# Kernel optimization log

Hardware: AMD Instinct MI355X
Metric: run time of the kernel (lower is better)

## Reference

```python
import jax, jax.numpy as jnp
import numpy as np

E = 256        # HP.EMBED_SIZE
R = 8          # number of derivation rules / MLPs
S = 512        # number of sequential derivation steps
N = 256        # nodes produced per step
N_INIT = 1024  # initial axiom (thax) embeddings
TOTAL = N_INIT + S * N  # 132096 rows in the vectors buffer
M = 65536      # masked nodes fed to eval_net


def setup_inputs() -> dict:
    key = jax.random.key(0)
    ks = jax.random.split(key, 12)
    rng = np.random.default_rng(0)

    init_vecs = jax.random.normal(ks[0], (N_INIT, E), jnp.float32)
    # rule MLPs: concat(2 parents) -> E (relu) -> E
    W1 = jax.random.normal(ks[1], (R, 2 * E, E), jnp.float32) * (1.0 / np.sqrt(2 * E))
    b1 = jnp.zeros((R, E), jnp.float32)
    W2 = jax.random.normal(ks[2], (R, E, E), jnp.float32) * (1.0 / np.sqrt(E))
    b2 = jnp.zeros((R, E), jnp.float32)
    # eval net: E -> E (relu) -> 1
    eval_W1 = jax.random.normal(ks[3], (E, E), jnp.float32) * (1.0 / np.sqrt(E))
    eval_b1 = jnp.zeros((E,), jnp.float32)
    eval_W2 = jax.random.normal(ks[4], (E, 1), jnp.float32) * (1.0 / np.sqrt(E))
    eval_b2 = jnp.zeros((1,), jnp.float32)

    # step s writes rows [N_INIT + s*N, N_INIT + (s+1)*N)
    ind_steps = (N_INIT + np.arange(S * N, dtype=np.int32)).reshape(S, N)
    # parents drawn causally from already-computed prefix [0, N_INIT + s*N)
    highs = (N_INIT + np.arange(S, dtype=np.int64) * N)[:, None, None]
    pars_ind_steps = (rng.random((S, N, 2)) * highs).astype(np.int32)
    rule_steps = rng.integers(0, R, size=(S,)).astype(np.int32)
    mask = rng.integers(0, TOTAL, size=(M,)).astype(np.int32)

    pos = jax.random.uniform(ks[5], (M,), jnp.float32)
    neg = jax.random.uniform(ks[6], (M,), jnp.float32)
    target = jnp.round(jax.random.uniform(ks[7], (M,), jnp.float32))

    return {
        'init_vecs': init_vecs, 'W1': W1, 'b1': b1, 'W2': W2, 'b2': b2,
        'eval_W1': eval_W1, 'eval_b1': eval_b1, 'eval_W2': eval_W2, 'eval_b2': eval_b2,
        'pos': pos, 'neg': neg, 'target': target,
        'ind_steps': jnp.asarray(ind_steps), 'pars_ind_steps': jnp.asarray(pars_ind_steps),
        'rule_steps': jnp.asarray(rule_steps), 'mask': jnp.asarray(mask),
    }


def reference(init_vecs, W1, b1, W2, b2, eval_W1, eval_b1, eval_W2, eval_b2,
              pos, neg, target, ind_steps, pars_ind_steps, rule_steps, mask):
    vectors = jnp.zeros((TOTAL, E), init_vecs.dtype).at[:N_INIT].set(init_vecs)

    def step(vec, xs):
        inds, pars, r = xs            # [N], [N,2], scalar rule id
        p = vec[pars].reshape(N, 2 * E)   # gather parents
        h = jax.nn.relu(p @ W1[r] + b1[r])
        out = h @ W2[r] + b2[r]
        return vec.at[inds].set(out), None  # scatter new node embeddings

    vectors, _ = jax.lax.scan(step, vectors, (ind_steps, pars_ind_steps, rule_steps))

    x = vectors[mask]
    val = (jax.nn.relu(x @ eval_W1 + eval_b1) @ eval_W2 + eval_b2)[:, 0]

    # pos_weight = POS_WEIGHT_EXTRA * tot_neg / tot_pos (constant w.r.t. grads)
    pw = jax.lax.stop_gradient(jnp.sum(neg) / jnp.maximum(jnp.sum(pos), 1.0))
    # BCEWithLogitsLoss(pos_weight, reduction='none')
    contrib = pw * target * jax.nn.softplus(-val) + (1.0 - target) * jax.nn.softplus(val)
    loss = jnp.sum((pos + neg) * contrib)
    posOK = jnp.sum(pos * (val >= 0))
    negOK = jnp.sum(neg * (val < 0))
    return loss, posOK, negOK
```

## Files before the change

kernel.cpp:

```cpp
#include <hip/hip_runtime.h>
#include <math.h>

#define EMB   256
#define TWOE  512
#define NINIT 1024
#define NSTEP 512
#define NPS   256
#define TOTAL (NINIT + NSTEP * NPS)
#define MM    65536
#define NNODE (NSTEP * NPS)
#define NKEY  2048
#define BTH   512
#define TROWS 32
#define CHK_SH  16384
#define RULE_SH (24 * CHK_SH)

typedef short s16x8 __attribute__((ext_vector_type(8)));
typedef float f32x4 __attribute__((ext_vector_type(4)));

#define OFF_VECH   0ull
#define OFF_VECL   ((size_t)TOTAL * EMB * 2)
#define OFF_VAL    (2ull * (size_t)TOTAL * EMB * 2)
#define OFF_CNT    (OFF_VAL + (size_t)MM * 4)
#define OFF_ACC    (OFF_CNT + 4096)
#define OFF_KCNT   (OFF_ACC + 256)
#define OFF_KOFS   (OFF_KCNT + (size_t)NKEY * 4)
#define OFF_NL     (OFF_KOFS + (size_t)NKEY * 4)
#define OFF_TPL    (OFF_NL + 256)
#define OFF_BROWS  (OFF_TPL + 4096)
#define OFF_WSPLIT (OFF_BROWS + (size_t)NNODE * 4)


__device__ __forceinline__ void store_dev_u32(unsigned* p, unsigned v) {
  asm volatile("global_store_dword %0, %1, off sc0 sc1" :: "v"(p), "v"(v) : "memory");
}
__device__ __forceinline__ void store_dev_b64(void* p, uint2 v) {
  asm volatile("global_store_dwordx2 %0, %1, off sc0 sc1" :: "v"(p), "v"(v) : "memory");
}
__device__ __forceinline__ void store_dev_b128(void* p, uint4 v) {
  store_dev_b64(p, make_uint2(v.x, v.y));
  store_dev_b64((char*)p + 8, make_uint2(v.z, v.w));
}
__device__ __forceinline__ unsigned load_dev_u32(const unsigned* p) {
  unsigned r;
  asm volatile("global_load_dword %0, %1, off sc0 sc1\n\ts_waitcnt vmcnt(0)"
               : "=v"(r) : "v"(p) : "memory");
  return r;
}

__device__ __forceinline__ void split8(const float* f, uint4& h4, uint4& l4) {
  unsigned hu[8], lu[8];
  #pragma unroll
  for (int i = 0; i < 8; ++i) {
    unsigned u = __builtin_bit_cast(unsigned, f[i]);
    float rh = __builtin_bit_cast(float, u & 0xffff0000u);
    float rl = f[i] - rh;
    hu[i] = u >> 16;
    lu[i] = __builtin_bit_cast(unsigned, rl) >> 16;
  }
  h4 = make_uint4(hu[0] | (hu[1] << 16), hu[2] | (hu[3] << 16),
                  hu[4] | (hu[5] << 16), hu[6] | (hu[7] << 16));
  l4 = make_uint4(lu[0] | (lu[1] << 16), lu[2] | (lu[3] << 16),
                  lu[4] | (lu[5] << 16), lu[6] | (lu[7] << 16));
}
__device__ __forceinline__ void split1(float f, short& hi, short& lo) {
  unsigned u = __builtin_bit_cast(unsigned, f);
  float rh = __builtin_bit_cast(float, u & 0xffff0000u);
  float rl = f - rh;
  hi = (short)(u >> 16);
  lo = (short)(__builtin_bit_cast(unsigned, rl) >> 16);
}

__global__ void zero_scratch(unsigned* done, double* acc) {
  if (threadIdx.x < 256) done[threadIdx.x] = 0u;
  if (threadIdx.x < 8) acc[threadIdx.x] = 0.0;
}

__global__ void init_convert(const float* __restrict__ src,
                             unsigned short* __restrict__ vh,
                             unsigned short* __restrict__ vl) {
  int slot = blockIdx.x * blockDim.x + threadIdx.x;
  float f[8];
  *(float4*)&f[0] = reinterpret_cast<const float4*>(src)[slot * 2];
  *(float4*)&f[4] = reinterpret_cast<const float4*>(src)[slot * 2 + 1];
  uint4 h4, l4;
  split8(f, h4, l4);
  *(uint4*)(vh + (size_t)slot * 8) = h4;
  *(uint4*)(vl + (size_t)slot * 8) = l4;
}

__global__ __launch_bounds__(512)
void presplit(const float* __restrict__ W1, const float* __restrict__ W2,
              short* __restrict__ Ws)
{
  const int blk = blockIdx.x;
  const int r = blk / 24, c = blk % 24;
  const float* src; int kbase;
  if (c < 16) { src = W1 + (size_t)r * TWOE * EMB; kbase = c * 32; }
  else        { src = W2 + (size_t)r * EMB * EMB;  kbase = (c - 16) * 32; }
  short* dst = Ws + (size_t)blk * CHK_SH;
  const int tid = threadIdx.x;
  #pragma unroll
  for (int u = 0; u < 2; ++u) {
    int qq = tid + u * 512;
    int g = qq >> 6, l = qq & 63;
    const float* p = src + (size_t)(kbase + ((l >> 4) << 3)) * EMB + (g << 4) + (l & 15);
    float f[8];
    #pragma unroll
    for (int i = 0; i < 8; ++i) f[i] = p[i * EMB];
    uint4 h4, l4;
    split8(f, h4, l4);
    *(uint4*)(dst + (size_t)qq * 8) = h4;
    *(uint4*)(dst + 8192 + (size_t)qq * 8) = l4;
  }
}

__global__ __launch_bounds__(1024)
void prepass(const int* __restrict__ pars, const int* __restrict__ rules,
             int* __restrict__ kcnt, int* __restrict__ kofs,
             int* __restrict__ brows, int* __restrict__ tpl, int* __restrict__ nlp)
{
  __shared__ unsigned char slvl[TOTAL];
  __shared__ int scnt[NKEY];
  __shared__ int sofs[NKEY];
  __shared__ int swmax[16];
  const int t = threadIdx.x;
  for (int i = t; i < NINIT; i += 1024) slvl[i] = 0;
  for (int k = t; k < NKEY; k += 1024) scnt[k] = 0;
  __syncthreads();
  int Pa[8], Pb[8];
  if (t < NPS) {
    #pragma unroll
    for (int w = 0; w < 8; ++w) {
      Pa[w] = pars[2 * (w * NPS + t)];
      Pb[w] = pars[2 * (w * NPS + t) + 1];
    }
  }
  int lmax = 0;
  for (int s0 = 0; s0 < NSTEP; s0 += 8) {
    int Na[8], Nb[8];
    if (t < NPS && s0 + 8 < NSTEP) {
      #pragma unroll
      for (int w = 0; w < 8; ++w) {
        Na[w] = pars[2 * ((s0 + 8 + w) * NPS + t)];
        Nb[w] = pars[2 * ((s0 + 8 + w) * NPS + t) + 1];
      }
    }
    #pragma unroll
    for (int w = 0; w < 8; ++w) {
      if (t < NPS) {
        int l1 = slvl[Pa[w]], l2 = slvl[Pb[w]];
        int lv = 1 + (l1 > l2 ? l1 : l2);
        slvl[NINIT + (s0 + w) * NPS + t] = (unsigned char)lv;
        if (lv > lmax) lmax = lv;
      }
      __syncthreads();
    }
    if (t < NPS && s0 + 8 < NSTEP) {
      #pragma unroll
      for (int w = 0; w < 8; ++w) { Pa[w] = Na[w]; Pb[w] = Nb[w]; }
    }
  }
  for (int o = 32; o; o >>= 1) lmax = max(lmax, __shfl_down(lmax, o));
  if ((t & 63) == 0) swmax[t >> 6] = lmax;
  __syncthreads();
  if (t == 0) {
    int m = 0;
    for (int w = 0; w < 16; ++w) m = max(m, swmax[w]);
    nlp[0] = m;
  }
  for (int i = t; i < NNODE; i += 1024) {
    int key = (int)slvl[NINIT + i] * 8 + rules[i >> 8];
    atomicAdd(&scnt[key], 1);
  }
  __syncthreads();
  if (t == 0) {
    int run = 0;
    for (int k = 0; k < NKEY; ++k) {
      sofs[k] = run; kofs[k] = run; kcnt[k] = scnt[k]; run += scnt[k];
    }
  }
  __syncthreads();
  if (t < 256) {
    int s = 0;
    #pragma unroll
    for (int r = 0; r < 8; ++r) s += (scnt[t * 8 + r] + TROWS - 1) >> 5;
    tpl[t] = s;
  }
  for (int i = t; i < NNODE; i += 1024) {
    int key = (int)slvl[NINIT + i] * 8 + rules[i >> 8];
    int pos = atomicAdd(&sofs[key], 1);
    brows[pos] = i;
  }
}

#define LOADW(S0, S1, S2, S3, ch) { \
  const short* cs_ = Wr + (size_t)(ch) * CHK_SH; \
  S0 = *(const uint4*)(cs_ + (size_t)tid * 8); \
  S1 = *(const uint4*)(cs_ + (size_t)(512 + tid) * 8); \
  S2 = *(const uint4*)(cs_ + 8192 + (size_t)tid * 8); \
  S3 = *(const uint4*)(cs_ + 8192 + (size_t)(512 + tid) * 8); }
#define WRITEW(buf, S0, S1, S2, S3) { \
  *(uint4*)&wB[buf][tid * 8] = S0; \
  *(uint4*)&wB[buf][(512 + tid) * 8] = S1; \
  *(uint4*)&wB[buf][8192 + tid * 8] = S2; \
  *(uint4*)&wB[buf][8192 + (512 + tid) * 8] = S3; }

__global__ __launch_bounds__(BTH, 1)
void scan_kernel(const short* __restrict__ Ws, const float* __restrict__ b1,
                 const float* __restrict__ b2, const int* __restrict__ pars,
                 unsigned short* __restrict__ vech, unsigned short* __restrict__ vecl,
                 const int* __restrict__ kcnt, const int* __restrict__ kofs,
                 const int* __restrict__ brows, const int* __restrict__ tpl,
                 const int* __restrict__ nlp, unsigned* __restrict__ done)
{
  __shared__ short wB[2][CHK_SH];
  __shared__ short hH[TROWS][264];
  __shared__ short hLo[TROWS][264];
  __shared__ int spar[2 * TROWS];
  __shared__ int sorow[TROWS];
  const int tid = threadIdx.x;
  const int bid = blockIdx.x;
  const int lane = tid & 63;
  const int w = tid >> 6;
  const int rw = w & 1, cwb = (w >> 1) << 2;
  const int row16 = lane & 15, kb8 = (lane >> 4) << 3;
  const int arow = (rw << 4) + row16;
  const int hrow = (rw << 4) + ((lane >> 4) << 2);
  const int NL = nlp[0];
  const int xcd = bid & 7, jb = bid >> 3;

  for (int lv = 1; lv <= NL; ++lv) {
    if (tid == 0 && lv > 1) {
      const unsigned need = (unsigned)tpl[lv - 1];
      const unsigned* dp = done + (lv - 1);
      while (load_dev_u32(dp) < need) __builtin_amdgcn_s_sleep(2);
    }
    __syncthreads();
    int cum[9]; cum[0] = 0;
    int cnts[8], ofss[8];
    #pragma unroll
    for (int r = 0; r < 8; ++r) {
      int c = kcnt[lv * 8 + r];
      cnts[r] = c; ofss[r] = kofs[lv * 8 + r];
      cum[r + 1] = cum[r] + ((c + TROWS - 1) >> 5);
    }
    const int G = cum[8];
    const int q = G >> 3, rm = G & 7;
    const int Gx = q + (xcd < rm ? 1 : 0);
    const int sx = xcd * q + (xcd < rm ? xcd : rm);
    for (int j = jb; j < Gx; j += 32) {
      const int g = sx + j;
      int rr = 0;
      while (g >= cum[rr + 1]) ++rr;
      const int t0 = g - cum[rr];
      const int cnt_b = cnts[rr], ofs_b = ofss[rr];
      const int tbase = t0 * TROWS;
      const short* __restrict__ Wr = Ws + (size_t)rr * RULE_SH;

      __syncthreads();
      if (tid < 2 * TROWS) {
        int slot = tbase + (tid >> 1);
        if (slot >= cnt_b) slot = cnt_b - 1;
        int node = brows[ofs_b + slot];
        spar[tid] = pars[2 * node + (tid & 1)];
        if ((tid & 1) == 0) sorow[tid >> 1] = NINIT + node;
      }
      uint4 sA0, sA1, sA2, sA3, sB0, sB1, sB2, sB3;
      LOADW(sA0, sA1, sA2, sA3, 0);
      __syncthreads();
      const int par0 = spar[2 * arow], par1 = spar[2 * arow + 1];
      float b1v[4], b2v[4];
      #pragma unroll
      for (int g4 = 0; g4 < 4; ++g4) {
        b1v[g4] = b1[rr * EMB + ((cwb + g4) << 4) + row16];
        b2v[g4] = b2[rr * EMB + ((cwb + g4) << 4) + row16];
      }
      uint4 ah[3], al[3];
      #pragma unroll
      for (int d = 0; d < 3; ++d) {
        int kg = d * 32 + kb8;
        int par = (kg >> 8) ? par1 : par0;
        size_t off = (size_t)par * EMB + (kg & 255);
        ah[d] = *(const uint4*)(vech + off);
        al[d] = *(const uint4*)(vecl + off);
      }
      WRITEW(0, sA0, sA1, sA2, sA3);
      LOADW(sB0, sB1, sB2, sB3, 1);
      __syncthreads();
      f32x4 acc[4]  = {{0,0,0,0},{0,0,0,0},{0,0,0,0},{0,0,0,0}};
      f32x4 acc2[4] = {{0,0,0,0},{0,0,0,0},{0,0,0,0},{0,0,0,0}};
      #pragma unroll
      for (int cc = 0; cc < 24; ++cc) {
        if (cc < 16) {
          s16x8 Ah = __builtin_bit_cast(s16x8, ah[cc % 3]);
          s16x8 Al = __builtin_bit_cast(s16x8, al[cc % 3]);
          #pragma unroll
          for (int g4 = 0; g4 < 4; ++g4) {
            int gi = (cwb + g4) * 64 + lane;
            s16x8 Bh = *(const s16x8*)&wB[cc & 1][gi * 8];
            s16x8 Bl = *(const s16x8*)&wB[cc & 1][8192 + gi * 8];
            acc[g4] = __builtin_amdgcn_mfma_f32_16x16x32_bf16(Ah, Bh, acc[g4], 0, 0, 0);
            acc[g4] = __builtin_amdgcn_mfma_f32_16x16x32_bf16(Ah, Bl, acc[g4], 0, 0, 0);
            acc[g4] = __builtin_amdgcn_mfma_f32_16x16x32_bf16(Al, Bh, acc[g4], 0, 0, 0);
          }
        } else {
          const int kc = (cc - 16) * 32 + kb8;
          s16x8 Ah = *(const s16x8*)&hH[arow][kc];
          s16x8 Al = *(const s16x8*)&hLo[arow][kc];
          #pragma unroll
          for (int g4 = 0; g4 < 4; ++g4) {
            int gi = (cwb + g4) * 64 + lane;
            s16x8 Bh = *(const s16x8*)&wB[cc & 1][gi * 8];
            s16x8 Bl = *(const s16x8*)&wB[cc & 1][8192 + gi * 8];
            acc2[g4] = __builtin_amdgcn_mfma_f32_16x16x32_bf16(Ah, Bh, acc2[g4], 0, 0, 0);
            acc2[g4] = __builtin_amdgcn_mfma_f32_16x16x32_bf16(Ah, Bl, acc2[g4], 0, 0, 0);
            acc2[g4] = __builtin_amdgcn_mfma_f32_16x16x32_bf16(Al, Bh, acc2[g4], 0, 0, 0);
          }
        }
        if (cc == 15) {
          #pragma unroll
          for (int g4 = 0; g4 < 4; ++g4) {
            #pragma unroll
            for (int jj = 0; jj < 4; ++jj) {
              int col = ((cwb + g4) << 4) + row16;
              short hi, lo;
              split1(fmaxf(acc[g4][jj] + b1v[g4], 0.f), hi, lo);
              hH[hrow + jj][col] = hi; hLo[hrow + jj][col] = lo;
            }
          }
        }
        if (cc < 23) {
          if (((cc + 1) & 1) == 0) { WRITEW(0, sA0, sA1, sA2, sA3); }
          else                     { WRITEW(1, sB0, sB1, sB2, sB3); }
        }
        if (cc < 22) {
          if (((cc + 2) & 1) == 0) { LOADW(sA0, sA1, sA2, sA3, cc + 2); }
          else                     { LOADW(sB0, sB1, sB2, sB3, cc + 2); }
        }
        if (cc + 3 <= 15) {
          int d = (cc + 3) % 3;
          int kg = (cc + 3) * 32 + kb8;
          int par = (kg >> 8) ? par1 : par0;
          size_t off = (size_t)par * EMB + (kg & 255);
          ah[d] = *(const uint4*)(vech + off);
          al[d] = *(const uint4*)(vecl + off);
        }
        __syncthreads();
      }
      #pragma unroll
      for (int g4 = 0; g4 < 4; ++g4) {
        #pragma unroll
        for (int jj = 0; jj < 4; ++jj) {
          int col = ((cwb + g4) << 4) + row16;
          short hi, lo;
          split1(acc2[g4][jj] + b2v[g4], hi, lo);
          hH[hrow + jj][col] = hi; hLo[hrow + jj][col] = lo;
        }
      }
      __syncthreads();
      #pragma unroll
      for (int u = 0; u < 2; ++u) {
        int s = tid + u * 512;
        int row = s >> 5, c8 = (s & 31) * 8;
        uint4 h4 = *(const uint4*)&hH[row][c8];
        uint4 l4 = *(const uint4*)&hLo[row][c8];
        if (tbase + row < cnt_b) {
          size_t off = (size_t)sorow[row] * EMB + c8;
          store_dev_b128(vech + off, h4);
          store_dev_b128(vecl + off, l4);
        }
      }
      asm volatile("s_waitcnt vmcnt(0)" ::: "memory");
      __syncthreads();
      if (tid == 0)
        __hip_atomic_fetch_add(done + lv, 1u, __ATOMIC_RELAXED, __HIP_MEMORY_SCOPE_AGENT);
    }
  }
}

__global__ void reduce_pn(const float* __restrict__ pos, const float* __restrict__ neg,
                          double* acc) {
  double sp = 0.0, sn = 0.0;
  for (int m = blockIdx.x * blockDim.x + threadIdx.x; m < MM; m += gridDim.x * blockDim.x) {
    sp += (double)pos[m]; sn += (double)neg[m];
  }
  for (int o = 32; o; o >>= 1) { sp += __shfl_down(sp, o); sn += __shfl_down(sn, o); }
  __shared__ double rp[4], rn[4];
  int wid = threadIdx.x >> 6, lane = threadIdx.x & 63;
  if (lane == 0) { rp[wid] = sp; rn[wid] = sn; }
  __syncthreads();
  if (threadIdx.x == 0) {
    double tp = 0.0, tn = 0.0;
    for (int w = 0; w < 4; ++w) { tp += rp[w]; tn += rn[w]; }
    atomicAdd(&acc[0], tp); atomicAdd(&acc[1], tn);
  }
}

__global__ __launch_bounds__(256)
void eval_kernel(const unsigned short* __restrict__ vh, const unsigned short* __restrict__ vl,
                 const int* __restrict__ mask,
                 const float* __restrict__ eW1, const float* __restrict__ eb1,
                 const float* __restrict__ eW2, const float* __restrict__ eb2,
                 float* __restrict__ val)
{
  __shared__ float xL[64][36];
  __shared__ float wLx[32][260];
  __shared__ int mrow[64];
  const int tid = threadIdx.x;
  const int a = tid >> 4, b = tid & 15;
  const int m0 = blockIdx.x * 64;
  if (tid < 64) mrow[tid] = mask[m0 + tid];
  __syncthreads();

  float acc[4][16];
  #pragma unroll
  for (int i = 0; i < 4; ++i)
    #pragma unroll
    for (int j = 0; j < 16; ++j) acc[i][j] = 0.f;

  for (int c = 0; c < 8; ++c) {
    const int e0 = c * 32;
    for (int idx = tid; idx < 64 * 4; idx += 256) {
      int rr = idx >> 2, u = idx & 3;
      size_t off = (size_t)mrow[rr] * EMB + e0 + u * 8;
      uint4 hv = *(const uint4*)(vh + off);
      uint4 lv = *(const uint4*)(vl + off);
      const unsigned* hu = (const unsigned*)&hv;
      const unsigned* lu = (const unsigned*)&lv;
      float fo[8];
      #pragma unroll
      for (int jj = 0; jj < 4; ++jj) {
        fo[2 * jj] = __builtin_bit_cast(float, (hu[jj] & 0xffffu) << 16) +
                     __builtin_bit_cast(float, (lu[jj] & 0xffffu) << 16);
        fo[2 * jj + 1] = __builtin_bit_cast(float, hu[jj] & 0xffff0000u) +
                         __builtin_bit_cast(float, lu[jj] & 0xffff0000u);
      }
      *(float4*)&xL[rr][u * 8] = *(float4*)&fo[0];
      *(float4*)&xL[rr][u * 8 + 4] = *(float4*)&fo[4];
    }
    for (int idx = tid; idx < 32 * 64; idx += 256) {
      int e = idx >> 6, k4 = idx & 63;
      reinterpret_cast<float4*>(&wLx[e][0])[k4] =
          reinterpret_cast<const float4*>(eW1 + (size_t)(e0 + e) * EMB)[k4];
    }
    __syncthreads();
    #pragma unroll 4
    for (int e = 0; e < 32; ++e) {
      float xs[4];
      #pragma unroll
      for (int rr = 0; rr < 4; ++rr) xs[rr] = xL[a * 4 + rr][e];
      const float4* wr = reinterpret_cast<const float4*>(&wLx[e][0]) + b * 4;
      float wk[16];
      *reinterpret_cast<float4*>(&wk[0])  = wr[0];
      *reinterpret_cast<float4*>(&wk[4])  = wr[1];
      *reinterpret_cast<float4*>(&wk[8])  = wr[2];
      *reinterpret_cast<float4*>(&wk[12]) = wr[3];
      #pragma unroll
      for (int rr = 0; rr < 4; ++rr)
        #pragma unroll
        for (int kk = 0; kk < 16; ++kk)
          acc[rr][kk] = fmaf(xs[rr], wk[kk], acc[rr][kk]);
    }
    __syncthreads();
  }

  float eb2v = eb2[0];
  float pv[4];
  #pragma unroll
  for (int rr = 0; rr < 4; ++rr) {
    float s = 0.f;
    #pragma unroll
    for (int kk = 0; kk < 16; ++kk) {
      float h = acc[rr][kk] + eb1[b * 16 + kk];
      h = fmaxf(h, 0.f);
      s += h * eW2[b * 16 + kk];
    }
    pv[rr] = s;
  }
  #pragma unroll
  for (int m = 1; m < 16; m <<= 1) {
    #pragma unroll
    for (int rr = 0; rr < 4; ++rr) pv[rr] += __shfl_xor(pv[rr], m);
  }
  if (b == 0) {
    #pragma unroll
    for (int rr = 0; rr < 4; ++rr) val[m0 + a * 4 + rr] = pv[rr] + eb2v;
  }
}

__global__ void loss_kernel(const float* __restrict__ val, const float* __restrict__ pos,
                            const float* __restrict__ neg, const float* __restrict__ tgt,
                            double* acc)
{
  const float pw = (float)(acc[1] / fmax(acc[0], 1.0));
  double l = 0.0, pk = 0.0, nk = 0.0;
  for (int m = blockIdx.x * blockDim.x + threadIdx.x; m < MM; m += gridDim.x * blockDim.x) {
    float v = val[m], p = pos[m], n = neg[m], t = tgt[m];
    float lp = log1pf(expf(-fabsf(v)));
    float spn = fmaxf(-v, 0.f) + lp;
    float spp = fmaxf(v, 0.f) + lp;
    float contrib = pw * t * spn + (1.f - t) * spp;
    l += (double)((p + n) * contrib);
    if (v >= 0.f) pk += (double)p; else nk += (double)n;
  }
  for (int o = 32; o; o >>= 1) {
    l += __shfl_down(l, o); pk += __shfl_down(pk, o); nk += __shfl_down(nk, o);
  }
  __shared__ double s0[4], s1[4], s2[4];
  int wid = threadIdx.x >> 6, lane = threadIdx.x & 63;
  if (lane == 0) { s0[wid] = l; s1[wid] = pk; s2[wid] = nk; }
  __syncthreads();
  if (threadIdx.x == 0) {
    double ta = 0.0, tb = 0.0, tc = 0.0;
    for (int w = 0; w < 4; ++w) { ta += s0[w]; tb += s1[w]; tc += s2[w]; }
    atomicAdd(&acc[2], ta); atomicAdd(&acc[3], tb); atomicAdd(&acc[4], tc);
  }
}

__global__ void writeout(const double* __restrict__ acc, float* __restrict__ out) {
  if (threadIdx.x == 0) {
    out[0] = (float)acc[2];
    out[1] = (float)acc[3];
    out[2] = (float)acc[4];
  }
}

extern "C" void kernel_launch(void* const* d_in, const int* in_sizes, int n_in,
                              void* d_out, int out_size, void* d_ws, size_t ws_size,
                              hipStream_t stream)
{
  (void)in_sizes; (void)n_in; (void)out_size; (void)ws_size;
  const float* init_vecs = (const float*)d_in[0];
  const float* W1  = (const float*)d_in[1];
  const float* b1  = (const float*)d_in[2];
  const float* W2  = (const float*)d_in[3];
  const float* b2  = (const float*)d_in[4];
  const float* eW1 = (const float*)d_in[5];
  const float* eb1 = (const float*)d_in[6];
  const float* eW2 = (const float*)d_in[7];
  const float* eb2 = (const float*)d_in[8];
  const float* pos = (const float*)d_in[9];
  const float* neg = (const float*)d_in[10];
  const float* tgt = (const float*)d_in[11];
  const int* pars  = (const int*)d_in[13];
  const int* rules = (const int*)d_in[14];
  const int* mask  = (const int*)d_in[15];

  char* ws = (char*)d_ws;
  unsigned short* vech = (unsigned short*)(ws + OFF_VECH);
  unsigned short* vecl = (unsigned short*)(ws + OFF_VECL);
  float*    val   = (float*)(ws + OFF_VAL);
  unsigned* done  = (unsigned*)(ws + OFF_CNT);
  double*   acc   = (double*)(ws + OFF_ACC);
  int*      kcnt  = (int*)(ws + OFF_KCNT);
  int*      kofs  = (int*)(ws + OFF_KOFS);
  int*      nlp   = (int*)(ws + OFF_NL);
  int*      tpl   = (int*)(ws + OFF_TPL);
  int*      brows = (int*)(ws + OFF_BROWS);
  short*    Ws    = (short*)(ws + OFF_WSPLIT);

  zero_scratch<<<1, 256, 0, stream>>>(done, acc);
  prepass<<<1, 1024, 0, stream>>>(pars, rules, kcnt, kofs, brows, tpl, nlp);
  init_convert<<<128, 256, 0, stream>>>(init_vecs, vech, vecl);
  presplit<<<192, 512, 0, stream>>>(W1, W2, Ws);
  scan_kernel<<<256, BTH, 0, stream>>>(Ws, b1, b2, pars, vech, vecl,
                                       kcnt, kofs, brows, tpl, nlp, done);
  reduce_pn<<<128, 256, 0, stream>>>(pos, neg, acc);
  eval_kernel<<<1024, 256, 0, stream>>>(vech, vecl, mask, eW1, eb1, eW2, eb2, val);
  loss_kernel<<<128, 256, 0, stream>>>(val, pos, neg, tgt, acc);
  writeout<<<1, 1, 0, stream>>>(acc, (float*)d_out);
}
```

Baseline: 1.115 ms.

## Stream weight chunks into LDS with direct global-to-LDS loads, triple-buffered

Replaces the register-staged weight double buffer (global load into VGPRs, then LDS write) with direct global_load_lds transfers into a three-slot LDS ring, two chunks ahead. Hand-tuned s_waitcnt vmcnt counts plus raw barriers replace __syncthreads, so loads stay in flight across iterations. This removes the VGPR staging registers and the LDS write instructions. In exchange it uses more LDS and depends on fragile vmcnt counting that must match the gather loads issued in each iteration.

```diff
diff --git a/kernel.cpp b/kernel.cpp
--- a/kernel.cpp
+++ b/kernel.cpp
@@ -48,6 +48,17 @@
   return r;
 }
 
+__device__ __forceinline__ void wait_vm_lgkm(int n) {
+  switch (n) {
+    case 0:  asm volatile("s_waitcnt vmcnt(0) lgkmcnt(0)"  ::: "memory"); break;
+    case 4:  asm volatile("s_waitcnt vmcnt(4) lgkmcnt(0)"  ::: "memory"); break;
+    case 6:  asm volatile("s_waitcnt vmcnt(6) lgkmcnt(0)"  ::: "memory"); break;
+    case 8:  asm volatile("s_waitcnt vmcnt(8) lgkmcnt(0)"  ::: "memory"); break;
+    case 10: asm volatile("s_waitcnt vmcnt(10) lgkmcnt(0)" ::: "memory"); break;
+    default: asm volatile("s_waitcnt vmcnt(12) lgkmcnt(0)" ::: "memory"); break;
+  }
+}
+
 __device__ __forceinline__ void split8(const float* f, uint4& h4, uint4& l4) {
   unsigned hu[8], lu[8];
   #pragma unroll
@@ -69,6 +80,17 @@
   float rl = f - rh;
   hi = (short)(u >> 16);
   lo = (short)(__builtin_bit_cast(unsigned, rl) >> 16);
+}
+
+__device__ __forceinline__ void stage_chunk(short* ldst, const short* gsrc,
+                                            int w, int lane) {
+  #pragma unroll
+  for (int i = 0; i < 4; ++i) {
+    int off = (w * 4 + i) * 512;
+    __builtin_amdgcn_global_load_lds(
+        (const __attribute__((address_space(1))) unsigned int*)(gsrc + off + lane * 8),
+        (__attribute__((address_space(3))) unsigned int*)(ldst + off), 16, 0, 0);
+  }
 }
 
 __global__ void zero_scratch(unsigned* done, double* acc) {
@@ -194,18 +216,6 @@
   }
 }
 
-#define LOADW(S0, S1, S2, S3, ch) { \
-  const short* cs_ = Wr + (size_t)(ch) * CHK_SH; \
-  S0 = *(const uint4*)(cs_ + (size_t)tid * 8); \
-  S1 = *(const uint4*)(cs_ + (size_t)(512 + tid) * 8); \
-  S2 = *(const uint4*)(cs_ + 8192 + (size_t)tid * 8); \
-  S3 = *(const uint4*)(cs_ + 8192 + (size_t)(512 + tid) * 8); }
-#define WRITEW(buf, S0, S1, S2, S3) { \
-  *(uint4*)&wB[buf][tid * 8] = S0; \
-  *(uint4*)&wB[buf][(512 + tid) * 8] = S1; \
-  *(uint4*)&wB[buf][8192 + tid * 8] = S2; \
-  *(uint4*)&wB[buf][8192 + (512 + tid) * 8] = S3; }
-
 __global__ __launch_bounds__(BTH, 1)
 void scan_kernel(const short* __restrict__ Ws, const float* __restrict__ b1,
                  const float* __restrict__ b2, const int* __restrict__ pars,
@@ -214,7 +224,7 @@
                  const int* __restrict__ brows, const int* __restrict__ tpl,
                  const int* __restrict__ nlp, unsigned* __restrict__ done)
 {
-  __shared__ short wB[2][CHK_SH];
+  __shared__ short wR[3][CHK_SH];
   __shared__ short hH[TROWS][264];
   __shared__ short hLo[TROWS][264];
   __shared__ int spar[2 * TROWS];
@@ -259,6 +269,8 @@
       const short* __restrict__ Wr = Ws + (size_t)rr * RULE_SH;
 
       __syncthreads();
+      stage_chunk(&wR[0][0], Wr, w, lane);
+      stage_chunk(&wR[1][0], Wr + CHK_SH, w, lane);
       if (tid < 2 * TROWS) {
         int slot = tbase + (tid >> 1);
         if (slot >= cnt_b) slot = cnt_b - 1;
@@ -266,8 +278,6 @@
         spar[tid] = pars[2 * node + (tid & 1)];
         if ((tid & 1) == 0) sorow[tid >> 1] = NINIT + node;
       }
-      uint4 sA0, sA1, sA2, sA3, sB0, sB1, sB2, sB3;
-      LOADW(sA0, sA1, sA2, sA3, 0);
       __syncthreads();
       const int par0 = spar[2 * arow], par1 = spar[2 * arow + 1];
       float b1v[4], b2v[4];
@@ -285,24 +295,49 @@
         ah[d] = *(const uint4*)(vech + off);
         al[d] = *(const uint4*)(vecl + off);
       }
-      WRITEW(0, sA0, sA1, sA2, sA3);
-      LOADW(sB0, sB1, sB2, sB3, 1);
-      __syncthreads();
       f32x4 acc[4]  = {{0,0,0,0},{0,0,0,0},{0,0,0,0},{0,0,0,0}};
       f32x4 acc2[4] = {{0,0,0,0},{0,0,0,0},{0,0,0,0},{0,0,0,0}};
       #pragma unroll
       for (int cc = 0; cc < 24; ++cc) {
+        {
+          const int n = (cc == 0) ? 10 : (cc == 1) ? 12 :
+                        (cc <= 13) ? 8 : (cc == 14) ? 6 : (cc <= 22) ? 4 : 0;
+          wait_vm_lgkm(n);
+        }
+        __builtin_amdgcn_s_barrier();
+        if (cc + 2 < 24)
+          stage_chunk(&wR[(cc + 2) % 3][0], Wr + (size_t)(cc + 2) * CHK_SH, w, lane);
+        if (cc + 3 <= 15) {
+          int d = (cc + 3) % 3;
+          int kg = (cc + 3) * 32 + kb8;
+          int par = (kg >> 8) ? par1 : par0;
+          size_t off = (size_t)par * EMB + (kg & 255);
+          ah[d] = *(const uint4*)(vech + off);
+          al[d] = *(const uint4*)(vecl + off);
+        }
         if (cc < 16) {
           s16x8 Ah = __builtin_bit_cast(s16x8, ah[cc % 3]);
           s16x8 Al = __builtin_bit_cast(s16x8, al[cc % 3]);
           #pragma unroll
           for (int g4 = 0; g4 < 4; ++g4) {
             int gi = (cwb + g4) * 64 + lane;
-            s16x8 Bh = *(const s16x8*)&wB[cc & 1][gi * 8];
-            s16x8 Bl = *(const s16x8*)&wB[cc & 1][8192 + gi * 8];
+            s16x8 Bh = *(const s16x8*)&wR[cc % 3][gi * 8];
+            s16x8 Bl = *(const s16x8*)&wR[cc % 3][8192 + gi * 8];
             acc[g4] = __builtin_amdgcn_mfma_f32_16x16x32_bf16(Ah, Bh, acc[g4], 0, 0, 0);
             acc[g4] = __builtin_amdgcn_mfma_f32_16x16x32_bf16(Ah, Bl, acc[g4], 0, 0, 0);
             acc[g4] = __builtin_amdgcn_mfma_f32_16x16x32_bf16(Al, Bh, acc[g4], 0, 0, 0);
+          }
+          if (cc == 15) {
+            #pragma unroll
+            for (int g4 = 0; g4 < 4; ++g4) {
+              #pragma unroll
+              for (int jj = 0; jj < 4; ++jj) {
+                int col = ((cwb + g4) << 4) + row16;
+                short hi, lo;
+                split1(fmaxf(acc[g4][jj] + b1v[g4], 0.f), hi, lo);
+                hH[hrow + jj][col] = hi; hLo[hrow + jj][col] = lo;
+              }
+            }
           }
         } else {
           const int kc = (cc - 16) * 32 + kb8;
@@ -311,43 +346,15 @@
           #pragma unroll
           for (int g4 = 0; g4 < 4; ++g4) {
             int gi = (cwb + g4) * 64 + lane;
-            s16x8 Bh = *(const s16x8*)&wB[cc & 1][gi * 8];
-            s16x8 Bl = *(const s16x8*)&wB[cc & 1][8192 + gi * 8];
+            s16x8 Bh = *(const s16x8*)&wR[cc % 3][gi * 8];
+            s16x8 Bl = *(const s16x8*)&wR[cc % 3][8192 + gi * 8];
             acc2[g4] = __builtin_amdgcn_mfma_f32_16x16x32_bf16(Ah, Bh, acc2[g4], 0, 0, 0);
             acc2[g4] = __builtin_amdgcn_mfma_f32_16x16x32_bf16(Ah, Bl, acc2[g4], 0, 0, 0);
             acc2[g4] = __builtin_amdgcn_mfma_f32_16x16x32_bf16(Al, Bh, acc2[g4], 0, 0, 0);
           }
         }
-        if (cc == 15) {
-          #pragma unroll
-          for (int g4 = 0; g4 < 4; ++g4) {
-            #pragma unroll
-            for (int jj = 0; jj < 4; ++jj) {
-              int col = ((cwb + g4) << 4) + row16;
-              short hi, lo;
-              split1(fmaxf(acc[g4][jj] + b1v[g4], 0.f), hi, lo);
-              hH[hrow + jj][col] = hi; hLo[hrow + jj][col] = lo;
-            }
-          }
-        }
-        if (cc < 23) {
-          if (((cc + 1) & 1) == 0) { WRITEW(0, sA0, sA1, sA2, sA3); }
-          else                     { WRITEW(1, sB0, sB1, sB2, sB3); }
-        }
-        if (cc < 22) {
-          if (((cc + 2) & 1) == 0) { LOADW(sA0, sA1, sA2, sA3, cc + 2); }
-          else                     { LOADW(sB0, sB1, sB2, sB3, cc + 2); }
-        }
-        if (cc + 3 <= 15) {
-          int d = (cc + 3) % 3;
-          int kg = (cc + 3) * 32 + kb8;
-          int par = (kg >> 8) ? par1 : par0;
-          size_t off = (size_t)par * EMB + (kg & 255);
-          ah[d] = *(const uint4*)(vech + off);
-          al[d] = *(const uint4*)(vecl + off);
-        }
-        __syncthreads();
-      }
+      }
+      __syncthreads();
       #pragma unroll
       for (int g4 = 0; g4 < 4; ++g4) {
         #pragma unroll
```

Measured after the change: 1.264 ms. 1.13x slower.
